# Kernel tuning notes

Hardware: AMD Instinct MI355X
Metric: run time of the kernel (lower is better)

The kernel has to match this reference:

```python
import jax, jax.numpy as jnp
import numpy as np

SLOPE = 0.01  # torch LeakyReLU default negative_slope

def lrelu(x):
    return jax.nn.leaky_relu(x, SLOPE)

def rgcn_conv(x, edge_index, edge_type, rel_w, root_w, bias, num_relations=2):
    # PyG RGCNConv: out = x @ root + bias + sum_r mean_{edges of rel r into i}(x_j @ W_r)
    N = x.shape[0]
    src, dst = edge_index[0], edge_index[1]
    out = x @ root_w + bias
    # transform once per relation at node level, then gather per edge
    h = jnp.einsum('nd,rde->rne', x, rel_w)          # [R, N, d]
    msg = h[edge_type, src]                           # [E, d] single gather
    for r in range(num_relations):
        m = (edge_type == r)
        s = jax.ops.segment_sum(jnp.where(m[:, None], msg, 0.0), dst, num_segments=N)
        cnt = jax.ops.segment_sum(m.astype(x.dtype), dst, num_segments=N)
        out = out + s / jnp.maximum(cnt, 1.0)[:, None]  # mean aggregation (0 if no edges)
    return out


def setup_inputs() -> dict:
    key = jax.random.key(0)
    ks = jax.random.split(key, 24)
    N, E, H = 50000, 800000, 256
    Q = H // 4
    def lin(k, i, o):
        k1, k2 = jax.random.split(k)
        s = 1.0 / np.sqrt(i)
        return (jax.random.uniform(k1, (i, o), jnp.float32, -s, s),
                jax.random.uniform(k2, (o,), jnp.float32, -s, s))
    Wd, bd = lin(ks[0], 768, Q)
    Wt, bt = lin(ks[1], 768, Q)
    Wn, bn = lin(ks[2], 5, Q)
    Wc, bc = lin(ks[3], 3, Q)
    Wi, bi = lin(ks[4], H, H)
    Wo1, bo1 = lin(ks[5], H, H)
    Wo2, bo2 = lin(ks[6], H, 2)
    s = 1.0 / np.sqrt(H)
    rel_w1 = jax.random.uniform(ks[7], (2, H, H), jnp.float32, -s, s)
    root_w1 = jax.random.uniform(ks[8], (H, H), jnp.float32, -s, s)
    bias1 = jnp.zeros((H,), jnp.float32)
    rel_w2 = jax.random.uniform(ks[9], (2, H, H), jnp.float32, -s, s)
    root_w2 = jax.random.uniform(ks[10], (H, H), jnp.float32, -s, s)
    bias2 = jnp.zeros((H,), jnp.float32)
    return {
        'des': jax.random.normal(ks[11], (N, 768), jnp.float32),
        'tweet': jax.random.normal(ks[12], (N, 768), jnp.float32),
        'num_prop': jax.random.normal(ks[13], (N, 5), jnp.float32),
        'cat_prop': jax.random.normal(ks[14], (N, 3), jnp.float32),
        'edge_index': jax.random.randint(ks[15], (2, E), 0, N, jnp.int32),
        'edge_type': jax.random.randint(ks[16], (E,), 0, 2, jnp.int32),
        'Wd': Wd, 'bd': bd, 'Wt': Wt, 'bt': bt, 'Wn': Wn, 'bn': bn, 'Wc': Wc, 'bc': bc,
        'Wi': Wi, 'bi': bi,
        'rel_w1': rel_w1, 'root_w1': root_w1, 'bias1': bias1,
        'rel_w2': rel_w2, 'root_w2': root_w2, 'bias2': bias2,
        'Wo1': Wo1, 'bo1': bo1, 'Wo2': Wo2, 'bo2': bo2,
    }


def reference(des, tweet, num_prop, cat_prop, edge_index, edge_type,
              Wd, bd, Wt, bt, Wn, bn, Wc, bc, Wi, bi,
              rel_w1, root_w1, bias1, rel_w2, root_w2, bias2,
              Wo1, bo1, Wo2, bo2):
    # dropout is identity in eval mode
    d = lrelu(des @ Wd + bd)
    t = lrelu(tweet @ Wt + bt)
    n = lrelu(num_prop @ Wn + bn)
    c = lrelu(cat_prop @ Wc + bc)
    x = jnp.concatenate([d, t, n, c], axis=1)           # [N, H]
    x = lrelu(x @ Wi + bi)
    x = rgcn_conv(x, edge_index, edge_type, rel_w1, root_w1, bias1)
    x = rgcn_conv(x, edge_index, edge_type, rel_w2, root_w2, bias2)
    x = lrelu(x @ Wo1 + bo1)
    return x @ Wo2 + bo2                                 # [N, 2]
```

## Files before the change

kernel.cpp:

```cpp
#include <hip/hip_runtime.h>
#include <stdint.h>

__device__ __forceinline__ float bf2f(unsigned short h) {
    union { unsigned int u; float f; } x;
    x.u = ((unsigned int)h) << 16;
    return x.f;
}
__device__ __forceinline__ unsigned short f2bf(float f) {
    union { float f; unsigned int u; } x;
    x.f = f;
    unsigned int u = x.u;
    unsigned int r = (u + 0x7FFFu + ((u >> 16) & 1u)) >> 16;
    return (unsigned short)r;
}
__device__ __forceinline__ float ldf(const void* p, size_t i, int f32) {
    return f32 ? ((const float*)p)[i] : bf2f(((const unsigned short*)p)[i]);
}

typedef __attribute__((ext_vector_type(8))) short short8;
typedef __attribute__((ext_vector_type(4))) float floatx4;

__global__ void k_detect(const unsigned short* __restrict__ p, int* flag) {
    __shared__ int cnt;
    if (threadIdx.x == 0) cnt = 0;
    __syncthreads();
    int c = 0;
    for (int i = threadIdx.x; i < 4096; i += 256) {
        unsigned e = (p[i] >> 7) & 0xFFu;
        if (e >= 0xC0u) c++;
    }
    atomicAdd(&cnt, c);
    __syncthreads();
    if (threadIdx.x == 0) *flag = (cnt > 32) ? 1 : 0;
}

template <int BN>
__global__ __launch_bounds__(256) void gemm_nt(
    const void* __restrict__ A0, const void* __restrict__ A1,
    const void* __restrict__ A2, int o0, int o1, int o2, int lda,
    const unsigned short* __restrict__ Bt, int ldb,
    unsigned short* __restrict__ C, int ldc,
    const unsigned short* __restrict__ bias,
    int M, int K, int act, const int* __restrict__ dflag)
{
    constexpr int BM = 128, BK = 64;
    constexpr int NJ = (BN == 128) ? 4 : 2;
    const int af32 = dflag ? *dflag : 0;
    const int tid  = threadIdx.x;
    const int wave = tid >> 6;
    const int lane = tid & 63;
    const int quad = lane >> 4;
    const int l16  = lane & 15;
    const int m0   = blockIdx.x * BM;
    const int n0   = blockIdx.y * BN;
    const int wm   = (wave & 1) * 64;
    const int wn   = (wave >> 1) * (BN / 2);

    __shared__ short8 As[8 * (BM + 2)];
    __shared__ short8 Bs[8 * (BN + 2)];

    floatx4 acc[4][NJ];
#pragma unroll
    for (int i = 0; i < 4; i++)
#pragma unroll
        for (int j = 0; j < NJ; j++) acc[i][j] = (floatx4){0.f, 0.f, 0.f, 0.f};

    for (int kt = 0; kt < K; kt += BK) {
        const void* Ap = (kt < 256) ? A0 : (kt < 512) ? A1 : A2;
        const int Ao = (kt < 256) ? o0 : (kt < 512) ? o1 : o2;
        const int ko = kt & 255;
#pragma unroll
        for (int c = 0; c < 4; c++) {
            int lin = c * 256 + tid;
            int row = lin >> 3, kq = lin & 7;
            int gr = m0 + row; if (gr > M - 1) gr = M - 1;
            size_t eoff = (size_t)gr * lda + Ao + ko + kq * 8;
            short8 v;
            if (af32) {
                const float* pf = (const float*)Ap + eoff;
#pragma unroll
                for (int z = 0; z < 8; z++) v[z] = (short)f2bf(pf[z]);
            } else {
                v = *(const short8*)((const unsigned short*)Ap + eoff);
            }
            As[kq * (BM + 2) + row] = v;
        }
#pragma unroll
        for (int c = 0; c < (BN * 8) / 256; c++) {
            int lin = c * 256 + tid;
            int n = lin >> 3, kq = lin & 7;
            short8 v = *(const short8*)(Bt + (size_t)(n0 + n) * ldb + kt + kq * 8);
            Bs[kq * (BN + 2) + n] = v;
        }
        __syncthreads();
#pragma unroll
        for (int s = 0; s < 2; s++) {
            short8 af[4], bfr[NJ];
#pragma unroll
            for (int i = 0; i < 4; i++)
                af[i] = As[(s * 4 + quad) * (BM + 2) + wm + i * 16 + l16];
#pragma unroll
            for (int j = 0; j < NJ; j++)
                bfr[j] = Bs[(s * 4 + quad) * (BN + 2) + wn + j * 16 + l16];
#pragma unroll
            for (int i = 0; i < 4; i++)
#pragma unroll
                for (int j = 0; j < NJ; j++)
                    acc[i][j] = __builtin_amdgcn_mfma_f32_16x16x32_bf16(
                        af[i], bfr[j], acc[i][j], 0, 0, 0);
        }
        __syncthreads();
    }

#pragma unroll
    for (int j = 0; j < NJ; j++) {
        int gc = n0 + wn + j * 16 + l16;
        float bv = bias ? bf2f(bias[gc]) : 0.f;
#pragma unroll
        for (int i = 0; i < 4; i++) {
            int grb = m0 + wm + i * 16 + quad * 4;
#pragma unroll
            for (int r = 0; r < 4; r++) {
                int gr = grb + r;
                if (gr < M) {
                    float v = acc[i][j][r] + bv;
                    if (act) v = v > 0.f ? v : 0.01f * v;
                    C[(size_t)gr * ldc + gc] = f2bf(v);
                }
            }
        }
    }
}

__global__ void t_cvt(const void* __restrict__ in, unsigned short* __restrict__ out,
                      int R, int C, const int* __restrict__ dflag) {
    int f32 = *dflag;
    int i = blockIdx.x * 256 + threadIdx.x;
    if (i < R * C) {
        int r = i / C, c = i % C;
        out[(size_t)c * R + r] = f2bf(ldf(in, i, f32));
    }
}

__global__ void build_bt(const void* __restrict__ root, const void* __restrict__ rel,
                         unsigned short* __restrict__ out, int H,
                         const int* __restrict__ dflag) {
    int f32 = *dflag;
    int i = blockIdx.x * 256 + threadIdx.x;
    int K3 = 3 * H;
    if (i < H * K3) {
        int k = i % K3;
        int n = i / K3;
        float v = (k < H) ? ldf(root, (size_t)k * H + n, f32)
                          : ldf(rel, (size_t)(k - H) * H + n, f32);
        out[i] = f2bf(v);
    }
}

__global__ void cvt_vec(const void* __restrict__ in, unsigned short* __restrict__ out,
                        int n, const int* __restrict__ dflag) {
    int f32 = *dflag;
    int i = blockIdx.x * 256 + threadIdx.x;
    if (i < n) out[i] = f2bf(ldf(in, i, f32));
}

__global__ void k_hist(const int* __restrict__ ei, const int* __restrict__ et,
                       int* cnt2, int N, int E) {
    int e = blockIdx.x * 256 + threadIdx.x;
    if (e < E) {
        int dst = ei[E + e];
        int t = et[e] & 1;
        if ((unsigned)dst < (unsigned)N) atomicAdd(&cnt2[t * N + dst], 1);
    }
}

__global__ void k_scan1(const int* __restrict__ cnt2, int* rowptr, int* bsum, int N) {
    __shared__ int sh[256];
    int t = threadIdx.x;
    int base = blockIdx.x * 1024 + t * 4;
    int v[4];
    int s = 0;
#pragma unroll
    for (int k = 0; k < 4; k++) {
        int idx = base + k;
        v[k] = (idx < N) ? (cnt2[idx] + cnt2[N + idx]) : 0;
        s += v[k];
    }
    sh[t] = s;
    __syncthreads();
    for (int off = 1; off < 256; off <<= 1) {
        int x = 0;
        if (t >= off) x = sh[t - off];
        __syncthreads();
        if (t >= off) sh[t] += x;
        __syncthreads();
    }
    int excl = sh[t] - s;
    int run = excl;
#pragma unroll
    for (int k = 0; k < 4; k++) {
        int idx = base + k;
        if (idx < N) rowptr[idx] = run;
        run += v[k];
    }
    if (t == 255) bsum[blockIdx.x] = sh[255];
}

__global__ void k_scan2(const int* __restrict__ bsum, int* bofs, int nb) {
    int t = threadIdx.x;
    int v = (t < nb) ? bsum[t] : 0;
    int orig = v;
    for (int off = 1; off < 64; off <<= 1) {
        int x = __shfl_up(v, off);
        if (t >= off) v += x;
    }
    if (t < nb) bofs[t] = v - orig;
}

__global__ void k_scan3(int* rowptr, const int* __restrict__ bofs, int N) {
    int i = blockIdx.x * 256 + threadIdx.x;
    if (i < N) rowptr[i] += bofs[i >> 10];
}

__global__ void k_fill(const int* __restrict__ ei, const int* __restrict__ et,
                       const int* __restrict__ rowptr, int* cursor, int* sorted,
                       int N, int E) {
    int e = blockIdx.x * 256 + threadIdx.x;
    if (e < E) {
        int src = ei[e];
        int dst = ei[E + e];
        int t = et[e] & 1;
        if ((unsigned)dst < (unsigned)N && (unsigned)src < (unsigned)N) {
            int pos = rowptr[dst] + atomicAdd(&cursor[dst], 1);
            sorted[pos] = src | (t << 24);
        }
    }
}

__global__ __launch_bounds__(256) void k_agg(
    const unsigned short* __restrict__ x,
    unsigned short* __restrict__ m0,
    unsigned short* __restrict__ m1,
    int N,
    const int* __restrict__ rowptr, const int* __restrict__ cnt2,
    const int* __restrict__ sorted)
{
    int wave = threadIdx.x >> 6;
    int lane = threadIdx.x & 63;
    int node = blockIdx.x * 4 + wave;
    if (node >= N) return;

    int start = rowptr[node];
    int c0 = cnt2[node], c1 = cnt2[N + node];
    int deg = c0 + c1;

    float a0[4] = {0.f, 0.f, 0.f, 0.f};
    float a1[4] = {0.f, 0.f, 0.f, 0.f};

    for (int b = 0; b < deg; b += 64) {
        int p = 0;
        if (b + lane < deg) p = sorted[start + b + lane];
        int cnt = deg - b; if (cnt > 64) cnt = 64;
        for (int j = 0; j < cnt; j++) {
            int q = __shfl(p, j);
            int src = q & 0xFFFFFF;
            if (src >= N) src = 0;
            const uint2* pr = (const uint2*)(x + (size_t)src * 256) + lane;
            uint2 raw = *pr;
            float v0 = bf2f((unsigned short)(raw.x & 0xFFFFu));
            float v1 = bf2f((unsigned short)(raw.x >> 16));
            float v2 = bf2f((unsigned short)(raw.y & 0xFFFFu));
            float v3 = bf2f((unsigned short)(raw.y >> 16));
            if ((q >> 24) == 0) { a0[0] += v0; a0[1] += v1; a0[2] += v2; a0[3] += v3; }
            else               { a1[0] += v0; a1[1] += v1; a1[2] += v2; a1[3] += v3; }
        }
    }
    float i0 = c0 > 0 ? 1.f / (float)c0 : 0.f;
    float i1 = c1 > 0 ? 1.f / (float)c1 : 0.f;
    uint2 o0, o1;
    o0.x = (unsigned int)f2bf(a0[0] * i0) | ((unsigned int)f2bf(a0[1] * i0) << 16);
    o0.y = (unsigned int)f2bf(a0[2] * i0) | ((unsigned int)f2bf(a0[3] * i0) << 16);
    o1.x = (unsigned int)f2bf(a1[0] * i1) | ((unsigned int)f2bf(a1[1] * i1) << 16);
    o1.y = (unsigned int)f2bf(a1[2] * i1) | ((unsigned int)f2bf(a1[3] * i1) << 16);
    *((uint2*)(m0 + (size_t)node * 256) + lane) = o0;
    *((uint2*)(m1 + (size_t)node * 256) + lane) = o1;
}

__global__ void k_small(const void* __restrict__ num, const void* __restrict__ cat,
                        const void* __restrict__ Wn, const void* __restrict__ bnp,
                        const void* __restrict__ Wc, const void* __restrict__ bcp,
                        unsigned short* __restrict__ xcat, int N,
                        const int* __restrict__ dflag)
{
    int f32 = *dflag;
    __shared__ float wn[320], wc[192], bns[64], bcs[64];
    int t = threadIdx.x;
    for (int i = t; i < 320; i += 256) wn[i] = ldf(Wn, i, f32);
    for (int i = t; i < 192; i += 256) wc[i] = ldf(Wc, i, f32);
    if (t < 64) { bns[t] = ldf(bnp, t, f32); bcs[t] = ldf(bcp, t, f32); }
    __syncthreads();

    int node = blockIdx.x * 128 + (t >> 1);
    int half = t & 1;
    if (node >= N) return;
    if (half == 0) {
        float in5[5];
#pragma unroll
        for (int i = 0; i < 5; i++) in5[i] = ldf(num, (size_t)node * 5 + i, f32);
        unsigned short* orow = xcat + (size_t)node * 256 + 128;
#pragma unroll 4
        for (int c = 0; c < 64; c++) {
            float v = bns[c];
#pragma unroll
            for (int i = 0; i < 5; i++) v += in5[i] * wn[i * 64 + c];
            v = v > 0.f ? v : 0.01f * v;
            orow[c] = f2bf(v);
        }
    } else {
        float in3[3];
#pragma unroll
        for (int i = 0; i < 3; i++) in3[i] = ldf(cat, (size_t)node * 3 + i, f32);
        unsigned short* orow = xcat + (size_t)node * 256 + 192;
#pragma unroll 4
        for (int c = 0; c < 64; c++) {
            float v = bcs[c];
#pragma unroll
            for (int i = 0; i < 3; i++) v += in3[i] * wc[i * 64 + c];
            v = v > 0.f ? v : 0.01f * v;
            orow[c] = f2bf(v);
        }
    }
}

__global__ __launch_bounds__(256) void k_final(
    const unsigned short* __restrict__ z,
    const void* __restrict__ Wo2, const void* __restrict__ bo2,
    void* __restrict__ out, int N, const int* __restrict__ dflag)
{
    int f32 = *dflag;
    __shared__ float w[512];
    int t = threadIdx.x;
    for (int i = t; i < 512; i += 256) w[i] = ldf(Wo2, i, f32);
    __syncthreads();
    int wave = t >> 6, lane = t & 63;
    int node = blockIdx.x * 4 + wave;
    if (node >= N) return;
    uint2 raw = *((const uint2*)(z + (size_t)node * 256) + lane);
    float v0 = bf2f((unsigned short)(raw.x & 0xFFFFu));
    float v1 = bf2f((unsigned short)(raw.x >> 16));
    float v2 = bf2f((unsigned short)(raw.y & 0xFFFFu));
    float v3 = bf2f((unsigned short)(raw.y >> 16));
    int k0 = lane * 4;
    float s0 = v0 * w[k0 * 2]     + v1 * w[(k0 + 1) * 2]     + v2 * w[(k0 + 2) * 2]     + v3 * w[(k0 + 3) * 2];
    float s1 = v0 * w[k0 * 2 + 1] + v1 * w[(k0 + 1) * 2 + 1] + v2 * w[(k0 + 2) * 2 + 1] + v3 * w[(k0 + 3) * 2 + 1];
    for (int off = 32; off; off >>= 1) {
        s0 += __shfl_xor(s0, off);
        s1 += __shfl_xor(s1, off);
    }
    if (lane == 0) {
        s0 += ldf(bo2, 0, f32);
        s1 += ldf(bo2, 1, f32);
        if (f32) {
            ((float*)out)[(size_t)node * 2]     = s0;
            ((float*)out)[(size_t)node * 2 + 1] = s1;
        } else {
            ((unsigned short*)out)[(size_t)node * 2]     = f2bf(s0);
            ((unsigned short*)out)[(size_t)node * 2 + 1] = f2bf(s1);
        }
    }
}

extern "C" void kernel_launch(void* const* d_in, const int* in_sizes, int n_in,
                              void* d_out, int out_size, void* d_ws, size_t ws_size,
                              hipStream_t stream)
{
    (void)n_in; (void)out_size; (void)ws_size;
    const void* des   = d_in[0];
    const void* tweet = d_in[1];
    const void* nump  = d_in[2];
    const void* catp  = d_in[3];
    const int*  ei    = (const int*)d_in[4];
    const int*  et    = (const int*)d_in[5];
    const void* Wd  = d_in[6];
    const void* bd  = d_in[7];
    const void* Wt  = d_in[8];
    const void* bt  = d_in[9];
    const void* Wn  = d_in[10];
    const void* bn  = d_in[11];
    const void* Wc  = d_in[12];
    const void* bc  = d_in[13];
    const void* Wi  = d_in[14];
    const void* bi  = d_in[15];
    const void* rel1  = d_in[16];
    const void* root1 = d_in[17];
    const void* bias1 = d_in[18];
    const void* rel2  = d_in[19];
    const void* root2 = d_in[20];
    const void* bias2 = d_in[21];
    const void* Wo1 = d_in[22];
    const void* bo1 = d_in[23];
    const void* Wo2 = d_in[24];
    const void* bo2 = d_in[25];

    const int N = in_sizes[0] / 768;
    const int E = in_sizes[5];

    char* ws = (char*)d_ws;
    size_t off = 0;
    auto alloc = [&](size_t bytes) -> char* {
        char* p = ws + off;
        off += (bytes + 255) & ~(size_t)255;
        return p;
    };
    unsigned short* B0 = (unsigned short*)alloc((size_t)N * 256 * 2);
    unsigned short* B1 = (unsigned short*)alloc((size_t)N * 256 * 2);
    unsigned short* B2 = (unsigned short*)alloc((size_t)N * 256 * 2);
    unsigned short* B3 = (unsigned short*)alloc((size_t)N * 256 * 2);
    unsigned short* WdT  = (unsigned short*)alloc(64 * 768 * 2);
    unsigned short* WtT  = (unsigned short*)alloc(64 * 768 * 2);
    unsigned short* WiT  = (unsigned short*)alloc(256 * 256 * 2);
    unsigned short* Wo1T = (unsigned short*)alloc(256 * 256 * 2);
    unsigned short* BT1  = (unsigned short*)alloc(256 * 768 * 2);
    unsigned short* BT2  = (unsigned short*)alloc(256 * 768 * 2);
    unsigned short* bias_bf = (unsigned short*)alloc(1152 * 2);
    unsigned short* bd_bf = bias_bf;
    unsigned short* bt_bf = bias_bf + 64;
    unsigned short* bi_bf = bias_bf + 128;
    unsigned short* b1_bf = bias_bf + 384;
    unsigned short* b2_bf = bias_bf + 640;
    unsigned short* bo1_bf = bias_bf + 896;
    int* dflag  = (int*)alloc(4);
    int* cnt2   = (int*)alloc((size_t)2 * N * 4);
    int* rowptr = (int*)alloc((size_t)(N + 1) * 4);
    int* cursor = (int*)alloc((size_t)N * 4);
    int* bsum   = (int*)alloc(64 * 4);
    int* bofs   = (int*)alloc(64 * 4);
    int* sorted = (int*)alloc((size_t)E * 4);

    size_t zlen = (size_t)(((char*)sorted + (size_t)E * 4) - (char*)cnt2);
    hipMemsetAsync(cnt2, 0, zlen, stream);

    k_detect<<<1, 256, 0, stream>>>((const unsigned short*)des, dflag);

    t_cvt<<<(768 * 64 + 255) / 256, 256, 0, stream>>>(Wd, WdT, 768, 64, dflag);
    t_cvt<<<(768 * 64 + 255) / 256, 256, 0, stream>>>(Wt, WtT, 768, 64, dflag);
    t_cvt<<<(256 * 256 + 255) / 256, 256, 0, stream>>>(Wi, WiT, 256, 256, dflag);
    t_cvt<<<(256 * 256 + 255) / 256, 256, 0, stream>>>(Wo1, Wo1T, 256, 256, dflag);
    build_bt<<<(256 * 768 + 255) / 256, 256, 0, stream>>>(root1, rel1, BT1, 256, dflag);
    build_bt<<<(256 * 768 + 255) / 256, 256, 0, stream>>>(root2, rel2, BT2, 256, dflag);
    cvt_vec<<<1, 256, 0, stream>>>(bd, bd_bf, 64, dflag);
    cvt_vec<<<1, 256, 0, stream>>>(bt, bt_bf, 64, dflag);
    cvt_vec<<<1, 256, 0, stream>>>(bi, bi_bf, 256, dflag);
    cvt_vec<<<1, 256, 0, stream>>>(bias1, b1_bf, 256, dflag);
    cvt_vec<<<1, 256, 0, stream>>>(bias2, b2_bf, 256, dflag);
    cvt_vec<<<1, 256, 0, stream>>>(bo1, bo1_bf, 256, dflag);

    int eb = (E + 255) / 256;
    k_hist<<<eb, 256, 0, stream>>>(ei, et, cnt2, N, E);
    int nb = (N + 1023) / 1024;
    k_scan1<<<nb, 256, 0, stream>>>(cnt2, rowptr, bsum, N);
    k_scan2<<<1, 64, 0, stream>>>(bsum, bofs, nb);
    k_scan3<<<(N + 255) / 256, 256, 0, stream>>>(rowptr, bofs, N);
    k_fill<<<eb, 256, 0, stream>>>(ei, et, rowptr, cursor, sorted, N, E);

    dim3 g64((N + 127) / 128, 1);
    gemm_nt<64><<<g64, 256, 0, stream>>>(des, des, des, 0, 256, 512, 768, WdT, 768,
                                         B0, 256, bd_bf, N, 768, 1, dflag);
    gemm_nt<64><<<g64, 256, 0, stream>>>(tweet, tweet, tweet, 0, 256, 512, 768, WtT, 768,
                                         B0 + 64, 256, bt_bf, N, 768, 1, dflag);
    k_small<<<(N + 127) / 128, 256, 0, stream>>>(nump, catp, Wn, bn, Wc, bc, B0, N, dflag);

    dim3 g128((N + 127) / 128, 2);
    gemm_nt<128><<<g128, 256, 0, stream>>>(B0, B0, B0, 0, 0, 0, 256, WiT, 256,
                                           B1, 256, bi_bf, N, 256, 1, nullptr);

    int ab = (N + 3) / 4;
    k_agg<<<ab, 256, 0, stream>>>(B1, B2, B3, N, rowptr, cnt2, sorted);
    gemm_nt<128><<<g128, 256, 0, stream>>>(B1, B2, B3, 0, 0, 0, 256, BT1, 768,
                                           B0, 256, b1_bf, N, 768, 0, nullptr);

    k_agg<<<ab, 256, 0, stream>>>(B0, B2, B3, N, rowptr, cnt2, sorted);
    gemm_nt<128><<<g128, 256, 0, stream>>>(B0, B2, B3, 0, 0, 0, 256, BT2, 768,
                                           B1, 256, b2_bf, N, 768, 0, nullptr);

    gemm_nt<128><<<g128, 256, 0, stream>>>(B1, B1, B1, 0, 0, 0, 256, Wo1T, 256,
                                           B0, 256, bo1_bf, N, 256, 1, nullptr);

    k_final<<<ab, 256, 0, stream>>>(B0, Wo2, bo2, d_out, N, dflag);
}
```

Measured before the change: 863.7 us.

## Merge encoder GEMMs, widen aggregation gathers, fuse bias kernels, shrink memset

Merges the two 768-wide encoder GEMMs (des and tweet) into a single launch, with blockIdx.y choosing the operand set. Loads fp32 A tiles as float4 pairs. Rewrites the edge aggregation so each half-wave handles a different edge using 16-byte loads, with the two halves combined by a cross-lane shuffle at the end. Also folds six bias-conversion launches into one kernel and narrows the memset to cover only the counters and cursor, not the sorted edge array. Together these aim to cut launch count, memset bandwidth and gather instruction count, in exchange for more registers and divergent branches in the aggregation kernel.

```diff
diff --git a/kernel.cpp b/kernel.cpp
--- a/kernel.cpp
+++ b/kernel.cpp
@@ -34,14 +34,16 @@
     if (threadIdx.x == 0) *flag = (cnt > 32) ? 1 : 0;
 }
 
-template <int BN>
+template <int BN, bool TWO>
 __global__ __launch_bounds__(256) void gemm_nt(
     const void* __restrict__ A0, const void* __restrict__ A1,
     const void* __restrict__ A2, int o0, int o1, int o2, int lda,
     const unsigned short* __restrict__ Bt, int ldb,
     unsigned short* __restrict__ C, int ldc,
     const unsigned short* __restrict__ bias,
-    int M, int K, int act, const int* __restrict__ dflag)
+    int M, int K, int act, const int* __restrict__ dflag,
+    const void* Ab = nullptr, const unsigned short* Btb = nullptr,
+    unsigned short* Cb = nullptr, const unsigned short* biasb = nullptr)
 {
     constexpr int BM = 128, BK = 64;
     constexpr int NJ = (BN == 128) ? 4 : 2;
@@ -52,9 +54,21 @@
     const int quad = lane >> 4;
     const int l16  = lane & 15;
     const int m0   = blockIdx.x * BM;
-    const int n0   = blockIdx.y * BN;
     const int wm   = (wave & 1) * 64;
     const int wn   = (wave >> 1) * (BN / 2);
+    int n0;
+    const unsigned short* BtS;
+    unsigned short* CS;
+    const unsigned short* biasS;
+    const void *A0S, *A1S, *A2S;
+    if (TWO && blockIdx.y == 1) {
+        n0 = 0; BtS = Btb; CS = Cb; biasS = biasb;
+        A0S = Ab; A1S = Ab; A2S = Ab;
+    } else {
+        n0 = TWO ? 0 : blockIdx.y * BN;
+        BtS = Bt; CS = C; biasS = bias;
+        A0S = A0; A1S = A1; A2S = A2;
+    }
 
     __shared__ short8 As[8 * (BM + 2)];
     __shared__ short8 Bs[8 * (BN + 2)];
@@ -66,7 +80,7 @@
         for (int j = 0; j < NJ; j++) acc[i][j] = (floatx4){0.f, 0.f, 0.f, 0.f};
 
     for (int kt = 0; kt < K; kt += BK) {
-        const void* Ap = (kt < 256) ? A0 : (kt < 512) ? A1 : A2;
+        const void* Ap = (kt < 256) ? A0S : (kt < 512) ? A1S : A2S;
         const int Ao = (kt < 256) ? o0 : (kt < 512) ? o1 : o2;
         const int ko = kt & 255;
 #pragma unroll
@@ -77,9 +91,13 @@
             size_t eoff = (size_t)gr * lda + Ao + ko + kq * 8;
             short8 v;
             if (af32) {
-                const float* pf = (const float*)Ap + eoff;
-#pragma unroll
-                for (int z = 0; z < 8; z++) v[z] = (short)f2bf(pf[z]);
+                const float4* pf = (const float4*)((const float*)Ap + eoff);
+                float4 f0 = pf[0];
+                float4 f1 = pf[1];
+                v[0] = (short)f2bf(f0.x); v[1] = (short)f2bf(f0.y);
+                v[2] = (short)f2bf(f0.z); v[3] = (short)f2bf(f0.w);
+                v[4] = (short)f2bf(f1.x); v[5] = (short)f2bf(f1.y);
+                v[6] = (short)f2bf(f1.z); v[7] = (short)f2bf(f1.w);
             } else {
                 v = *(const short8*)((const unsigned short*)Ap + eoff);
             }
@@ -89,7 +107,7 @@
         for (int c = 0; c < (BN * 8) / 256; c++) {
             int lin = c * 256 + tid;
             int n = lin >> 3, kq = lin & 7;
-            short8 v = *(const short8*)(Bt + (size_t)(n0 + n) * ldb + kt + kq * 8);
+            short8 v = *(const short8*)(BtS + (size_t)(n0 + n) * ldb + kt + kq * 8);
             Bs[kq * (BN + 2) + n] = v;
         }
         __syncthreads();
@@ -115,7 +133,7 @@
 #pragma unroll
     for (int j = 0; j < NJ; j++) {
         int gc = n0 + wn + j * 16 + l16;
-        float bv = bias ? bf2f(bias[gc]) : 0.f;
+        float bv = biasS ? bf2f(biasS[gc]) : 0.f;
 #pragma unroll
         for (int i = 0; i < 4; i++) {
             int grb = m0 + wm + i * 16 + quad * 4;
@@ -125,7 +143,7 @@
                 if (gr < M) {
                     float v = acc[i][j][r] + bv;
                     if (act) v = v > 0.f ? v : 0.01f * v;
-                    C[(size_t)gr * ldc + gc] = f2bf(v);
+                    CS[(size_t)gr * ldc + gc] = f2bf(v);
                 }
             }
         }
@@ -157,11 +175,20 @@
     }
 }
 
-__global__ void cvt_vec(const void* __restrict__ in, unsigned short* __restrict__ out,
-                        int n, const int* __restrict__ dflag) {
+__global__ void k_biases(const void* bd, const void* bt, const void* bi,
+                         const void* b1, const void* b2, const void* bo1,
+                         unsigned short* __restrict__ out, const int* __restrict__ dflag) {
     int f32 = *dflag;
-    int i = blockIdx.x * 256 + threadIdx.x;
-    if (i < n) out[i] = f2bf(ldf(in, i, f32));
+    for (int idx = threadIdx.x; idx < 1152; idx += 256) {
+        const void* p; int off;
+        if (idx < 64)       { p = bd;  off = idx; }
+        else if (idx < 128) { p = bt;  off = idx - 64; }
+        else if (idx < 384) { p = bi;  off = idx - 128; }
+        else if (idx < 640) { p = b1;  off = idx - 384; }
+        else if (idx < 896) { p = b2;  off = idx - 640; }
+        else                { p = bo1; off = idx - 896; }
+        out[idx] = f2bf(ldf(p, off, f32));
+    }
 }
 
 __global__ void k_hist(const int* __restrict__ ei, const int* __restrict__ et,
@@ -247,6 +274,8 @@
 {
     int wave = threadIdx.x >> 6;
     int lane = threadIdx.x & 63;
+    int half = lane >> 5;
+    int l32  = lane & 31;
     int node = blockIdx.x * 4 + wave;
     if (node >= N) return;
 
@@ -254,36 +283,76 @@
     int c0 = cnt2[node], c1 = cnt2[N + node];
     int deg = c0 + c1;
 
-    float a0[4] = {0.f, 0.f, 0.f, 0.f};
-    float a1[4] = {0.f, 0.f, 0.f, 0.f};
+    float a0[8] = {0,0,0,0,0,0,0,0};
+    float a1[8] = {0,0,0,0,0,0,0,0};
 
     for (int b = 0; b < deg; b += 64) {
+        int rem = deg - b; if (rem > 64) rem = 64;
         int p = 0;
-        if (b + lane < deg) p = sorted[start + b + lane];
-        int cnt = deg - b; if (cnt > 64) cnt = 64;
-        for (int j = 0; j < cnt; j++) {
-            int q = __shfl(p, j);
-            int src = q & 0xFFFFFF;
-            if (src >= N) src = 0;
-            const uint2* pr = (const uint2*)(x + (size_t)src * 256) + lane;
-            uint2 raw = *pr;
-            float v0 = bf2f((unsigned short)(raw.x & 0xFFFFu));
-            float v1 = bf2f((unsigned short)(raw.x >> 16));
-            float v2 = bf2f((unsigned short)(raw.y & 0xFFFFu));
-            float v3 = bf2f((unsigned short)(raw.y >> 16));
-            if ((q >> 24) == 0) { a0[0] += v0; a0[1] += v1; a0[2] += v2; a0[3] += v3; }
-            else               { a1[0] += v0; a1[1] += v1; a1[2] += v2; a1[3] += v3; }
-        }
+        if (lane < rem) p = sorted[start + b + lane];
+        int iters = (rem + 1) >> 1;
+        for (int t = 0; t < iters; t += 2) {
+            int e0 = 2 * t + half;
+            int e1 = e0 + 2;
+            int q0 = __shfl(p, e0 < 64 ? e0 : 63);
+            int q1 = __shfl(p, e1 < 64 ? e1 : 63);
+            bool v0ok = e0 < rem;
+            bool v1ok = e1 < rem;
+            int s0 = q0 & 0xFFFFFF; if (s0 >= N) s0 = 0;
+            int s1 = q1 & 0xFFFFFF; if (s1 >= N) s1 = 0;
+            uint4 r0 = *((const uint4*)(x + (size_t)s0 * 256) + l32);
+            uint4 r1 = *((const uint4*)(x + (size_t)s1 * 256) + l32);
+            if (v0ok) {
+                float f[8];
+                f[0] = bf2f((unsigned short)(r0.x & 0xFFFFu)); f[1] = bf2f((unsigned short)(r0.x >> 16));
+                f[2] = bf2f((unsigned short)(r0.y & 0xFFFFu)); f[3] = bf2f((unsigned short)(r0.y >> 16));
+                f[4] = bf2f((unsigned short)(r0.z & 0xFFFFu)); f[5] = bf2f((unsigned short)(r0.z >> 16));
+                f[6] = bf2f((unsigned short)(r0.w & 0xFFFFu)); f[7] = bf2f((unsigned short)(r0.w >> 16));
+                if ((q0 >> 24) & 1) {
+#pragma unroll
+                    for (int k = 0; k < 8; k++) a1[k] += f[k];
+                } else {
+#pragma unroll
+                    for (int k = 0; k < 8; k++) a0[k] += f[k];
+                }
+            }
+            if (v1ok) {
+                float f[8];
+                f[0] = bf2f((unsigned short)(r1.x & 0xFFFFu)); f[1] = bf2f((unsigned short)(r1.x >> 16));
+                f[2] = bf2f((unsigned short)(r1.y & 0xFFFFu)); f[3] = bf2f((unsigned short)(r1.y >> 16));
+                f[4] = bf2f((unsigned short)(r1.z & 0xFFFFu)); f[5] = bf2f((unsigned short)(r1.z >> 16));
+                f[6] = bf2f((unsigned short)(r1.w & 0xFFFFu)); f[7] = bf2f((unsigned short)(r1.w >> 16));
+                if ((q1 >> 24) & 1) {
+#pragma unroll
+                    for (int k = 0; k < 8; k++) a1[k] += f[k];
+                } else {
+#pragma unroll
+                    for (int k = 0; k < 8; k++) a0[k] += f[k];
+                }
+            }
+        }
+    }
+#pragma unroll
+    for (int k = 0; k < 8; k++) {
+        a0[k] += __shfl_xor(a0[k], 32);
+        a1[k] += __shfl_xor(a1[k], 32);
     }
     float i0 = c0 > 0 ? 1.f / (float)c0 : 0.f;
     float i1 = c1 > 0 ? 1.f / (float)c1 : 0.f;
-    uint2 o0, o1;
-    o0.x = (unsigned int)f2bf(a0[0] * i0) | ((unsigned int)f2bf(a0[1] * i0) << 16);
-    o0.y = (unsigned int)f2bf(a0[2] * i0) | ((unsigned int)f2bf(a0[3] * i0) << 16);
-    o1.x = (unsigned int)f2bf(a1[0] * i1) | ((unsigned int)f2bf(a1[1] * i1) << 16);
-    o1.y = (unsigned int)f2bf(a1[2] * i1) | ((unsigned int)f2bf(a1[3] * i1) << 16);
-    *((uint2*)(m0 + (size_t)node * 256) + lane) = o0;
-    *((uint2*)(m1 + (size_t)node * 256) + lane) = o1;
+    uint4 o;
+    if (half == 0) {
+        o.x = (unsigned)f2bf(a0[0] * i0) | ((unsigned)f2bf(a0[1] * i0) << 16);
+        o.y = (unsigned)f2bf(a0[2] * i0) | ((unsigned)f2bf(a0[3] * i0) << 16);
+        o.z = (unsigned)f2bf(a0[4] * i0) | ((unsigned)f2bf(a0[5] * i0) << 16);
+        o.w = (unsigned)f2bf(a0[6] * i0) | ((unsigned)f2bf(a0[7] * i0) << 16);
+        *((uint4*)(m0 + (size_t)node * 256) + l32) = o;
+    } else {
+        o.x = (unsigned)f2bf(a1[0] * i1) | ((unsigned)f2bf(a1[1] * i1) << 16);
+        o.y = (unsigned)f2bf(a1[2] * i1) | ((unsigned)f2bf(a1[3] * i1) << 16);
+        o.z = (unsigned)f2bf(a1[4] * i1) | ((unsigned)f2bf(a1[5] * i1) << 16);
+        o.w = (unsigned)f2bf(a1[6] * i1) | ((unsigned)f2bf(a1[7] * i1) << 16);
+        *((uint4*)(m1 + (size_t)node * 256) + l32) = o;
+    }
 }
 
 __global__ void k_small(const void* __restrict__ num, const void* __restrict__ cat,
@@ -431,13 +500,13 @@
     unsigned short* bo1_bf = bias_bf + 896;
     int* dflag  = (int*)alloc(4);
     int* cnt2   = (int*)alloc((size_t)2 * N * 4);
+    int* cursor = (int*)alloc((size_t)N * 4);
     int* rowptr = (int*)alloc((size_t)(N + 1) * 4);
-    int* cursor = (int*)alloc((size_t)N * 4);
     int* bsum   = (int*)alloc(64 * 4);
     int* bofs   = (int*)alloc(64 * 4);
     int* sorted = (int*)alloc((size_t)E * 4);
 
-    size_t zlen = (size_t)(((char*)sorted + (size_t)E * 4) - (char*)cnt2);
+    size_t zlen = (size_t)(((char*)cursor + (size_t)N * 4) - (char*)cnt2);
     hipMemsetAsync(cnt2, 0, zlen, stream);
 
     k_detect<<<1, 256, 0, stream>>>((const unsigned short*)des, dflag);
@@ -448,12 +517,7 @@
     t_cvt<<<(256 * 256 + 255) / 256, 256, 0, stream>>>(Wo1, Wo1T, 256, 256, dflag);
     build_bt<<<(256 * 768 + 255) / 256, 256, 0, stream>>>(root1, rel1, BT1, 256, dflag);
     build_bt<<<(256 * 768 + 255) / 256, 256, 0, stream>>>(root2, rel2, BT2, 256, dflag);
-    cvt_vec<<<1, 256, 0, stream>>>(bd, bd_bf, 64, dflag);
-    cvt_vec<<<1, 256, 0, stream>>>(bt, bt_bf, 64, dflag);
-    cvt_vec<<<1, 256, 0, stream>>>(bi, bi_bf, 256, dflag);
-    cvt_vec<<<1, 256, 0, stream>>>(bias1, b1_bf, 256, dflag);
-    cvt_vec<<<1, 256, 0, stream>>>(bias2, b2_bf, 256, dflag);
-    cvt_vec<<<1, 256, 0, stream>>>(bo1, bo1_bf, 256, dflag);
+    k_biases<<<1, 256, 0, stream>>>(bd, bt, bi, bias1, bias2, bo1, bias_bf, dflag);
 
     int eb = (E + 255) / 256;
     k_hist<<<eb, 256, 0, stream>>>(ei, et, cnt2, N, E);
@@ -463,28 +527,27 @@
     k_scan3<<<(N + 255) / 256, 256, 0, stream>>>(rowptr, bofs, N);
     k_fill<<<eb, 256, 0, stream>>>(ei, et, rowptr, cursor, sorted, N, E);
 
-    dim3 g64((N + 127) / 128, 1);
-    gemm_nt<64><<<g64, 256, 0, stream>>>(des, des, des, 0, 256, 512, 768, WdT, 768,
-                                         B0, 256, bd_bf, N, 768, 1, dflag);
-    gemm_nt<64><<<g64, 256, 0, stream>>>(tweet, tweet, tweet, 0, 256, 512, 768, WtT, 768,
-                                         B0 + 64, 256, bt_bf, N, 768, 1, dflag);
+    dim3 gEnc((N + 127) / 128, 2);
+    gemm_nt<64, true><<<gEnc, 256, 0, stream>>>(des, des, des, 0, 256, 512, 768,
+                                                WdT, 768, B0, 256, bd_bf, N, 768, 1, dflag,
+                                                tweet, WtT, B0 + 64, bt_bf);
     k_small<<<(N + 127) / 128, 256, 0, stream>>>(nump, catp, Wn, bn, Wc, bc, B0, N, dflag);
 
     dim3 g128((N + 127) / 128, 2);
-    gemm_nt<128><<<g128, 256, 0, stream>>>(B0, B0, B0, 0, 0, 0, 256, WiT, 256,
-                                           B1, 256, bi_bf, N, 256, 1, nullptr);
+    gemm_nt<128, false><<<g128, 256, 0, stream>>>(B0, B0, B0, 0, 0, 0, 256, WiT, 256,
+                                                  B1, 256, bi_bf, N, 256, 1, nullptr);
 
     int ab = (N + 3) / 4;
     k_agg<<<ab, 256, 0, stream>>>(B1, B2, B3, N, rowptr, cnt2, sorted);
-    gemm_nt<128><<<g128, 256, 0, stream>>>(B1, B2, B3, 0, 0, 0, 256, BT1, 768,
-                                           B0, 256, b1_bf, N, 768, 0, nullptr);
+    gemm_nt<128, false><<<g128, 256, 0, stream>>>(B1, B2, B3, 0, 0, 0, 256, BT1, 768,
+                                                  B0, 256, b1_bf, N, 768, 0, nullptr);
 
     k_agg<<<ab, 256, 0, stream>>>(B0, B2, B3, N, rowptr, cnt2, sorted);
-    gemm_nt<128><<<g128, 256, 0, stream>>>(B0, B2, B3, 0, 0, 0, 256, BT2, 768,
-                                           B1, 256, b2_bf, N, 768, 0, nullptr);
-
-    gemm_nt<128><<<g128, 256, 0, stream>>>(B1, B1, B1, 0, 0, 0, 256, Wo1T, 256,
-                                           B0, 256, bo1_bf, N, 256, 1, nullptr);
+    gemm_nt<128, false><<<g128, 256, 0, stream>>>(B0, B2, B3, 0, 0, 0, 256, BT2, 768,
+                                                  B1, 256, b2_bf, N, 768, 0, nullptr);
+
+    gemm_nt<128, false><<<g128, 256, 0, stream>>>(B1, B1, B1, 0, 0, 0, 256, Wo1T, 256,
+                                                  B0, 256, bo1_bf, N, 256, 1, nullptr);
 
     k_final<<<ab, 256, 0, stream>>>(B0, Wo2, bo2, d_out, N, dflag);
 }
```

Result: faster. 819.6 us (-5.1%).
